# Optimization experiments

Hardware: AMD Instinct MI355X
Metric: run time of the kernel (lower is better)

Reference implementation:

```python
import jax, jax.numpy as jnp
import numpy as np

H = 20  # hidden size (hard-coded in the module)

def setup_inputs() -> dict:
    key = jax.random.key(0)
    ks = jax.random.split(key, 7)
    B, T = 4096, 1000
    s = 1.0 / np.sqrt(H)  # torch default init bound for RNN/Linear
    x = jax.random.normal(ks[0], (B, T, 1), dtype=jnp.float32)
    W_ih = jax.random.uniform(ks[1], (H, 1), jnp.float32, -s, s)
    W_hh = jax.random.uniform(ks[2], (H, H), jnp.float32, -s, s)
    b_ih = jax.random.uniform(ks[3], (H,), jnp.float32, -s, s)
    b_hh = jax.random.uniform(ks[4], (H,), jnp.float32, -s, s)
    fc_w = jax.random.uniform(ks[5], (1, H), jnp.float32, -s, s)
    fc_b = jax.random.uniform(ks[6], (1,), jnp.float32, -s, s)
    return {"x": x, "W_ih": W_ih, "W_hh": W_hh, "b_ih": b_ih,
            "b_hh": b_hh, "fc_w": fc_w, "fc_b": fc_b}

def reference(x, W_ih, W_hh, b_ih, b_hh, fc_w, fc_b):
    # x: [B, T, 1] -> time-major [T, B, 1] for scan
    B = x.shape[0]
    xt = jnp.swapaxes(x, 0, 1)
    # precompute input projection for all timesteps: [T, B, H]
    xproj = jnp.einsum('tbi,hi->tbh', xt, W_ih) + b_ih + b_hh
    h0 = jnp.zeros((B, H), dtype=x.dtype)
    def step(h, xp_t):
        h_new = jax.nn.relu(xp_t + h @ W_hh.T)
        return h_new, None
    h_last, _ = jax.lax.scan(step, h0, xproj)
    # only the last hidden state feeds the head: fc1(rnn_out[:, -1, :])
    out = h_last @ fc_w.T + fc_b  # [B, 1]
    return out
```

## Files before the change

kernel.cpp:

```cpp
#include <hip/hip_runtime.h>


#define TT 1000

typedef float v2f __attribute__((ext_vector_type(2)));

struct Col { v2f p01, p23; float v4; };

struct Init { v2f i01, i23; float i4; };

#define PIN(v)  asm volatile("" : "+v"(v))
__device__ __forceinline__ void pinc(Col& c) {
    PIN(c.p01); PIN(c.p23); PIN(c.v4);
}
__device__ __forceinline__ void keepc(const Col& c) {
    asm volatile("" :: "v"(c.p01), "v"(c.p23), "v"(c.v4));
}

template <int CTRL>
__device__ __forceinline__ float dpp_f(float v) {
    return __int_as_float(__builtin_amdgcn_update_dpp(
        0, __float_as_int(v), CTRL, 0xF, 0xF, true));
}

#define QP_XOR1 0xB1
#define QP_XOR2 0x4E
#define ROR4   0x124
#define ROR8   0x128

__device__ __forceinline__ Init mkinit(v2f xs, float xt,
                                       const Col& w, const Col& b) {
    Init r;
    r.i01 = __builtin_elementwise_fma(xs, w.p01, b.p01);
    r.i23 = __builtin_elementwise_fma(xs, w.p23, b.p23);
    r.i4  = __builtin_fmaf(xt, w.v4, b.v4);
    return r;
}

template <int C1, int C2>
__device__ __forceinline__ void step(const Init& in,
                                     v2f& h01, v2f& h23, float& h4,
                                     const Col& wc0, const Col& wc1,
                                     const Col& wc2, const Col& wc3,
                                     const Col& wc4) {
    v2f  X01 = __builtin_elementwise_fma(h01.xx, wc0.p01, in.i01);
    v2f  X23 = __builtin_elementwise_fma(h01.xx, wc0.p23, in.i23);
    float x4 = __builtin_fmaf(h01.x, wc0.v4, in.i4);
    X01 = __builtin_elementwise_fma(h01.yy, wc1.p01, X01);
    X23 = __builtin_elementwise_fma(h01.yy, wc1.p23, X23);
    x4  = __builtin_fmaf(h01.y, wc1.v4, x4);

    v2f  Y01 = h23.xx * wc2.p01;
    v2f  Y23 = h23.xx * wc2.p23;
    float y4 = h23.x * wc2.v4;
    Y01 = __builtin_elementwise_fma(h23.yy, wc3.p01, Y01);
    Y23 = __builtin_elementwise_fma(h23.yy, wc3.p23, Y23);
    y4  = __builtin_fmaf(h23.y, wc3.v4, y4);
    { const v2f h4s = {h4, h4};
      Y01 = __builtin_elementwise_fma(h4s, wc4.p01, Y01);
      Y23 = __builtin_elementwise_fma(h4s, wc4.p23, Y23);
      y4  = __builtin_fmaf(h4, wc4.v4, y4); }

    const v2f z = {0.f, 0.f};

    {
        v2f A = X01 + Y01;
        float b0 = A.x, b1 = A.y;
        float t0 = dpp_f<C1>(b0), t1 = dpp_f<C1>(b1);
        b0 += t0; b1 += t1;
        t0 = dpp_f<C2>(b0); t1 = dpp_f<C2>(b1);
        b0 += t0; b1 += t1;
        v2f r = {b0, b1};
        h01 = __builtin_elementwise_max(r, z);
    }
    {
        v2f A = X23 + Y23;
        float b2 = A.x, b3 = A.y;
        float t2 = dpp_f<C1>(b2), t3 = dpp_f<C1>(b3);
        b2 += t2; b3 += t3;
        t2 = dpp_f<C2>(b2); t3 = dpp_f<C2>(b3);
        b2 += t2; b3 += t3;
        v2f r = {b2, b3};
        h23 = __builtin_elementwise_max(r, z);
    }
    {
        float b4 = x4 + y4;
        float t4 = dpp_f<C1>(b4); b4 += t4;
        t4 = dpp_f<C2>(b4); b4 += t4;
        h4 = fmaxf(b4, 0.f);
    }
}

__global__ void
__attribute__((amdgpu_flat_work_group_size(64, 64), amdgpu_waves_per_eu(1, 1)))
rnn_os_kernel(const float* __restrict__ x,
              const float* __restrict__ W_ih,
              const float* __restrict__ W_hh,
              const float* __restrict__ b_ih,
              const float* __restrict__ b_hh,
              const float* __restrict__ fc_w,
              const float* __restrict__ fc_b,
              float* __restrict__ out) {
    const int tid = blockIdx.x * 64 + threadIdx.x;
    const int b   = tid >> 4;
    const int gl  = tid & 15;
    const int a   = gl >> 2;
    const int bq  = gl & 3;

    Col we0, we1, we2, we3, we4;
    Col wo0, wo1, wo2, wo3, wo4;
#define LOADC(wk, k, rbase, cbase)                                            \
    { (wk).p01 = (v2f){ W_hh[((rbase) + 0) * 20 + (cbase) + (k)],             \
                        W_hh[((rbase) + 1) * 20 + (cbase) + (k)] };           \
      (wk).p23 = (v2f){ W_hh[((rbase) + 2) * 20 + (cbase) + (k)],             \
                        W_hh[((rbase) + 3) * 20 + (cbase) + (k)] };           \
      (wk).v4  =        W_hh[((rbase) + 4) * 20 + (cbase) + (k)]; }
    LOADC(we0, 0, a * 5, bq * 5) LOADC(we1, 1, a * 5, bq * 5)
    LOADC(we2, 2, a * 5, bq * 5) LOADC(we3, 3, a * 5, bq * 5)
    LOADC(we4, 4, a * 5, bq * 5)
    LOADC(wo0, 0, bq * 5, a * 5) LOADC(wo1, 1, bq * 5, a * 5)
    LOADC(wo2, 2, bq * 5, a * 5) LOADC(wo3, 3, bq * 5, a * 5)
    LOADC(wo4, 4, bq * 5, a * 5)
#undef LOADC

    const bool eact = (bq == 0);
    const bool oact = (a == 0);
    Col wie, bie, wio, bio;
#define LOADIB(wv, bv, base, act)                                             \
    { const float* pw = W_ih + (base);                                        \
      const float* p1 = b_ih + (base);                                        \
      const float* p2 = b_hh + (base);                                        \
      (wv).p01 = (v2f){ (act) ? pw[0] : 0.f, (act) ? pw[1] : 0.f };           \
      (wv).p23 = (v2f){ (act) ? pw[2] : 0.f, (act) ? pw[3] : 0.f };           \
      (wv).v4  =        (act) ? pw[4] : 0.f;                                  \
      (bv).p01 = (v2f){ (act) ? (p1[0] + p2[0]) : 0.f,                        \
                        (act) ? (p1[1] + p2[1]) : 0.f };                      \
      (bv).p23 = (v2f){ (act) ? (p1[2] + p2[2]) : 0.f,                        \
                        (act) ? (p1[3] + p2[3]) : 0.f };                      \
      (bv).v4  =        (act) ? (p1[4] + p2[4]) : 0.f; }
    LOADIB(wie, bie, a * 5,  eact)
    LOADIB(wio, bio, bq * 5, oact)
#undef LOADIB

    pinc(we0); pinc(we1); pinc(we2); pinc(we3); pinc(we4);
    pinc(wo0); pinc(wo1); pinc(wo2); pinc(wo3); pinc(wo4);
    pinc(wie); pinc(bie); pinc(wio); pinc(bio);

    v2f h01 = {0.f, 0.f}, h23 = {0.f, 0.f};
    float h4 = 0.f;

    const float* __restrict__ xb = x + (size_t)b * TT;

#define LOAD5(P, off)                                   \
    P##0 = *(const float4*)(xb + (off));                \
    P##1 = *(const float4*)(xb + (off) + 4);            \
    P##2 = *(const float4*)(xb + (off) + 8);            \
    P##3 = *(const float4*)(xb + (off) + 12);           \
    P##4 = *(const float4*)(xb + (off) + 16);

#define STEP_E(I) step<QP_XOR1, QP_XOR2>(I, h01, h23, h4, we0, we1, we2, we3, we4);
#define STEP_O(I) step<ROR4,    ROR8   >(I, h01, h23, h4, wo0, wo1, wo2, wo3, wo4);
#define RUN4(Q) {                                       \
        const v2f qlo = {Q.x, Q.y};                     \
        const v2f qhi = {Q.z, Q.w};                     \
        const Init iEL = mkinit(qlo.xx, qlo.x, wie, bie); \
        const Init iOL = mkinit(qlo.yy, qlo.y, wio, bio); \
        const Init iEH = mkinit(qhi.xx, qhi.x, wie, bie); \
        const Init iOH = mkinit(qhi.yy, qhi.y, wio, bio); \
        STEP_E(iEL) STEP_O(iOL)                         \
        STEP_E(iEH) STEP_O(iOH) }
#define RUN20(P) RUN4(P##0) RUN4(P##1) RUN4(P##2) RUN4(P##3) RUN4(P##4)

    float4 A0, A1, A2, A3, A4;
    float4 B0, B1, B2, B3, B4;
    LOAD5(A, 0)
    LOAD5(B, 20)

    for (int it = 0; it < 24; ++it) {
        const int base = it * 40;
        RUN20(A)
        LOAD5(A, base + 40)
        RUN20(B)
        LOAD5(B, base + 60)
    }
    RUN20(A)
    RUN20(B)

#undef RUN20
#undef RUN4
#undef STEP_E
#undef STEP_O
#undef LOAD5

    keepc(we0); keepc(we1); keepc(we2); keepc(we3); keepc(we4);
    keepc(wo0); keepc(wo1); keepc(wo2); keepc(wo3); keepc(wo4);
    keepc(wie); keepc(bie); keepc(wio); keepc(bio);

    float dot;
    {
        const float* pf = fc_w + bq * 5;
        float f0 = oact ? pf[0] : 0.f, f1 = oact ? pf[1] : 0.f;
        float f2 = oact ? pf[2] : 0.f, f3 = oact ? pf[3] : 0.f;
        float f4 = oact ? pf[4] : 0.f;
        dot = h01.x * f0;
        dot = __builtin_fmaf(h01.y, f1, dot);
        dot = __builtin_fmaf(h23.x, f2, dot);
        dot = __builtin_fmaf(h23.y, f3, dot);
        dot = __builtin_fmaf(h4,    f4, dot);
    }
    dot += __shfl_xor(dot, 1, 16);
    dot += __shfl_xor(dot, 2, 16);
    dot += __shfl_xor(dot, 4, 16);
    dot += __shfl_xor(dot, 8, 16);

    if (gl == 0)
        out[b] = dot + fc_b[0];
}

extern "C" void kernel_launch(void* const* d_in, const int* in_sizes, int n_in,
                              void* d_out, int out_size, void* d_ws, size_t ws_size,
                              hipStream_t stream) {
    const float* x    = (const float*)d_in[0];
    const float* W_ih = (const float*)d_in[1];
    const float* W_hh = (const float*)d_in[2];
    const float* b_ih = (const float*)d_in[3];
    const float* b_hh = (const float*)d_in[4];
    const float* fc_w = (const float*)d_in[5];
    const float* fc_b = (const float*)d_in[6];
    float* out = (float*)d_out;

    const int block = 64;
    const int grid  = (4096 * 16) / block;
    rnn_os_kernel<<<grid, block, 0, stream>>>(x, W_ih, W_hh, b_ih, b_hh,
                                              fc_w, fc_b, out);
}
```

Before: 152.2 us.

## Use eight lanes per batch row with bpermute hidden-state redistribution

```diff
diff --git a/kernel.cpp b/kernel.cpp
--- a/kernel.cpp
+++ b/kernel.cpp
@@ -17,19 +17,17 @@
     asm volatile("" :: "v"(c.p01), "v"(c.p23), "v"(c.v4));
 }
 
-template <int CTRL>
-__device__ __forceinline__ float dpp_f(float v) {
+__device__ __forceinline__ float dpp_xor1(float v) {
     return __int_as_float(__builtin_amdgcn_update_dpp(
-        0, __float_as_int(v), CTRL, 0xF, 0xF, true));
-}
-
-#define QP_XOR1 0xB1
-#define QP_XOR2 0x4E
-#define ROR4   0x124
-#define ROR8   0x128
-
-__device__ __forceinline__ Init mkinit(v2f xs, float xt,
-                                       const Col& w, const Col& b) {
+        0, __float_as_int(v), 0xB1, 0xF, 0xF, true));
+}
+
+__device__ __forceinline__ float bpf(int addr, float v) {
+    return __int_as_float(__builtin_amdgcn_ds_bpermute(addr, __float_as_int(v)));
+}
+
+__device__ __forceinline__ Init mkinit(float xt, const Col& w, const Col& b) {
+    const v2f xs = {xt, xt};
     Init r;
     r.i01 = __builtin_elementwise_fma(xs, w.p01, b.p01);
     r.i23 = __builtin_elementwise_fma(xs, w.p23, b.p23);
@@ -37,57 +35,72 @@
     return r;
 }
 
-template <int C1, int C2>
 __device__ __forceinline__ void step(const Init& in,
-                                     v2f& h01, v2f& h23, float& h4,
-                                     const Col& wc0, const Col& wc1,
-                                     const Col& wc2, const Col& wc3,
-                                     const Col& wc4) {
-    v2f  X01 = __builtin_elementwise_fma(h01.xx, wc0.p01, in.i01);
-    v2f  X23 = __builtin_elementwise_fma(h01.xx, wc0.p23, in.i23);
-    float x4 = __builtin_fmaf(h01.x, wc0.v4, in.i4);
-    X01 = __builtin_elementwise_fma(h01.yy, wc1.p01, X01);
-    X23 = __builtin_elementwise_fma(h01.yy, wc1.p23, X23);
-    x4  = __builtin_fmaf(h01.y, wc1.v4, x4);
-
-    v2f  Y01 = h23.xx * wc2.p01;
-    v2f  Y23 = h23.xx * wc2.p23;
-    float y4 = h23.x * wc2.v4;
-    Y01 = __builtin_elementwise_fma(h23.yy, wc3.p01, Y01);
-    Y23 = __builtin_elementwise_fma(h23.yy, wc3.p23, Y23);
-    y4  = __builtin_fmaf(h23.y, wc3.v4, y4);
-    { const v2f h4s = {h4, h4};
-      Y01 = __builtin_elementwise_fma(h4s, wc4.p01, Y01);
-      Y23 = __builtin_elementwise_fma(h4s, wc4.p23, Y23);
-      y4  = __builtin_fmaf(h4, wc4.v4, y4); }
+    v2f& h01, v2f& h23, float& h4,
+    v2f& hA01, v2f& hA23, float& hA4,
+    v2f& hB01, v2f& hB23, float& hB4,
+    int addrA, int addrB,
+    const Col& c0, const Col& c1, const Col& c2, const Col& c3, const Col& c4,
+    const Col& c5, const Col& c6, const Col& c7, const Col& c8, const Col& c9)
+{
+    v2f  X01 = __builtin_elementwise_fma(hA01.xx, c0.p01, in.i01);
+    v2f  X23 = __builtin_elementwise_fma(hA01.xx, c0.p23, in.i23);
+    float x4 = __builtin_fmaf(hA01.x, c0.v4, in.i4);
+    X01 = __builtin_elementwise_fma(hA01.yy, c1.p01, X01);
+    X23 = __builtin_elementwise_fma(hA01.yy, c1.p23, X23);
+    x4  = __builtin_fmaf(hA01.y, c1.v4, x4);
+    X01 = __builtin_elementwise_fma(hA23.xx, c2.p01, X01);
+    X23 = __builtin_elementwise_fma(hA23.xx, c2.p23, X23);
+    x4  = __builtin_fmaf(hA23.x, c2.v4, x4);
+    X01 = __builtin_elementwise_fma(hA23.yy, c3.p01, X01);
+    X23 = __builtin_elementwise_fma(hA23.yy, c3.p23, X23);
+    x4  = __builtin_fmaf(hA23.y, c3.v4, x4);
+    { const v2f s = {hA4, hA4};
+      X01 = __builtin_elementwise_fma(s, c4.p01, X01);
+      X23 = __builtin_elementwise_fma(s, c4.p23, X23);
+      x4  = __builtin_fmaf(hA4, c4.v4, x4); }
+
+    v2f  Y01 = hB01.xx * c5.p01;
+    v2f  Y23 = hB01.xx * c5.p23;
+    float y4 = hB01.x * c5.v4;
+    Y01 = __builtin_elementwise_fma(hB01.yy, c6.p01, Y01);
+    Y23 = __builtin_elementwise_fma(hB01.yy, c6.p23, Y23);
+    y4  = __builtin_fmaf(hB01.y, c6.v4, y4);
+    Y01 = __builtin_elementwise_fma(hB23.xx, c7.p01, Y01);
+    Y23 = __builtin_elementwise_fma(hB23.xx, c7.p23, Y23);
+    y4  = __builtin_fmaf(hB23.x, c7.v4, y4);
+    Y01 = __builtin_elementwise_fma(hB23.yy, c8.p01, Y01);
+    Y23 = __builtin_elementwise_fma(hB23.yy, c8.p23, Y23);
+    y4  = __builtin_fmaf(hB23.y, c8.v4, y4);
+    { const v2f s = {hB4, hB4};
+      Y01 = __builtin_elementwise_fma(s, c9.p01, Y01);
+      Y23 = __builtin_elementwise_fma(s, c9.p23, Y23);
+      y4  = __builtin_fmaf(hB4, c9.v4, y4); }
 
     const v2f z = {0.f, 0.f};
 
     {
         v2f A = X01 + Y01;
-        float b0 = A.x, b1 = A.y;
-        float t0 = dpp_f<C1>(b0), t1 = dpp_f<C1>(b1);
-        b0 += t0; b1 += t1;
-        t0 = dpp_f<C2>(b0); t1 = dpp_f<C2>(b1);
-        b0 += t0; b1 += t1;
-        v2f r = {b0, b1};
+        float t0 = dpp_xor1(A.x), t1 = dpp_xor1(A.y);
+        v2f r = {A.x + t0, A.y + t1};
         h01 = __builtin_elementwise_max(r, z);
+        hA01 = (v2f){ bpf(addrA, h01.x), bpf(addrA, h01.y) };
+        hB01 = (v2f){ bpf(addrB, h01.x), bpf(addrB, h01.y) };
     }
     {
         v2f A = X23 + Y23;
-        float b2 = A.x, b3 = A.y;
-        float t2 = dpp_f<C1>(b2), t3 = dpp_f<C1>(b3);
-        b2 += t2; b3 += t3;
-        t2 = dpp_f<C2>(b2); t3 = dpp_f<C2>(b3);
-        b2 += t2; b3 += t3;
-        v2f r = {b2, b3};
+        float t2 = dpp_xor1(A.x), t3 = dpp_xor1(A.y);
+        v2f r = {A.x + t2, A.y + t3};
         h23 = __builtin_elementwise_max(r, z);
+        hA23 = (v2f){ bpf(addrA, h23.x), bpf(addrA, h23.y) };
+        hB23 = (v2f){ bpf(addrB, h23.x), bpf(addrB, h23.y) };
     }
     {
         float b4 = x4 + y4;
-        float t4 = dpp_f<C1>(b4); b4 += t4;
-        t4 = dpp_f<C2>(b4); b4 += t4;
-        h4 = fmaxf(b4, 0.f);
+        float t4 = dpp_xor1(b4);
+        h4 = fmaxf(b4 + t4, 0.f);
+        hA4 = bpf(addrA, h4);
+        hB4 = bpf(addrB, h4);
     }
 }
 
@@ -102,52 +115,54 @@
               const float* __restrict__ fc_b,
               float* __restrict__ out) {
     const int tid = blockIdx.x * 64 + threadIdx.x;
-    const int b   = tid >> 4;
-    const int gl  = tid & 15;
-    const int a   = gl >> 2;
-    const int bq  = gl & 3;
-
-    Col we0, we1, we2, we3, we4;
-    Col wo0, wo1, wo2, wo3, wo4;
-#define LOADC(wk, k, rbase, cbase)                                            \
-    { (wk).p01 = (v2f){ W_hh[((rbase) + 0) * 20 + (cbase) + (k)],             \
-                        W_hh[((rbase) + 1) * 20 + (cbase) + (k)] };           \
-      (wk).p23 = (v2f){ W_hh[((rbase) + 2) * 20 + (cbase) + (k)],             \
-                        W_hh[((rbase) + 3) * 20 + (cbase) + (k)] };           \
-      (wk).v4  =        W_hh[((rbase) + 4) * 20 + (cbase) + (k)]; }
-    LOADC(we0, 0, a * 5, bq * 5) LOADC(we1, 1, a * 5, bq * 5)
-    LOADC(we2, 2, a * 5, bq * 5) LOADC(we3, 3, a * 5, bq * 5)
-    LOADC(we4, 4, a * 5, bq * 5)
-    LOADC(wo0, 0, bq * 5, a * 5) LOADC(wo1, 1, bq * 5, a * 5)
-    LOADC(wo2, 2, bq * 5, a * 5) LOADC(wo3, 3, bq * 5, a * 5)
-    LOADC(wo4, 4, bq * 5, a * 5)
+    const int b   = tid >> 3;
+    const int j   = tid & 7;
+    const int a   = j >> 1;
+    const int kh  = j & 1;
+
+    const int l      = threadIdx.x;
+    const int srcA   = (l & ~7) | (kh << 2);
+    const int addrA  = srcA << 2;
+    const int addrB  = addrA + 8;
+
+    Col c0, c1, c2, c3, c4, c5, c6, c7, c8, c9;
+#define LOADC(ck, k)                                                          \
+    { const int col = kh * 10 + (k);                                          \
+      (ck).p01 = (v2f){ W_hh[(a * 5 + 0) * 20 + col],                         \
+                        W_hh[(a * 5 + 1) * 20 + col] };                       \
+      (ck).p23 = (v2f){ W_hh[(a * 5 + 2) * 20 + col],                         \
+                        W_hh[(a * 5 + 3) * 20 + col] };                       \
+      (ck).v4  =        W_hh[(a * 5 + 4) * 20 + col]; }
+    LOADC(c0, 0) LOADC(c1, 1) LOADC(c2, 2) LOADC(c3, 3) LOADC(c4, 4)
+    LOADC(c5, 5) LOADC(c6, 6) LOADC(c7, 7) LOADC(c8, 8) LOADC(c9, 9)
 #undef LOADC
 
-    const bool eact = (bq == 0);
-    const bool oact = (a == 0);
-    Col wie, bie, wio, bio;
-#define LOADIB(wv, bv, base, act)                                             \
-    { const float* pw = W_ih + (base);                                        \
-      const float* p1 = b_ih + (base);                                        \
-      const float* p2 = b_hh + (base);                                        \
-      (wv).p01 = (v2f){ (act) ? pw[0] : 0.f, (act) ? pw[1] : 0.f };           \
-      (wv).p23 = (v2f){ (act) ? pw[2] : 0.f, (act) ? pw[3] : 0.f };           \
-      (wv).v4  =        (act) ? pw[4] : 0.f;                                  \
-      (bv).p01 = (v2f){ (act) ? (p1[0] + p2[0]) : 0.f,                        \
-                        (act) ? (p1[1] + p2[1]) : 0.f };                      \
-      (bv).p23 = (v2f){ (act) ? (p1[2] + p2[2]) : 0.f,                        \
-                        (act) ? (p1[3] + p2[3]) : 0.f };                      \
-      (bv).v4  =        (act) ? (p1[4] + p2[4]) : 0.f; }
-    LOADIB(wie, bie, a * 5,  eact)
-    LOADIB(wio, bio, bq * 5, oact)
-#undef LOADIB
-
-    pinc(we0); pinc(we1); pinc(we2); pinc(we3); pinc(we4);
-    pinc(wo0); pinc(wo1); pinc(wo2); pinc(wo3); pinc(wo4);
-    pinc(wie); pinc(bie); pinc(wio); pinc(bio);
+    const bool act = (kh == 0);
+    Col wie, bie;
+    {
+        const float* pw = W_ih + a * 5;
+        const float* p1 = b_ih + a * 5;
+        const float* p2 = b_hh + a * 5;
+        wie.p01 = (v2f){ act ? pw[0] : 0.f, act ? pw[1] : 0.f };
+        wie.p23 = (v2f){ act ? pw[2] : 0.f, act ? pw[3] : 0.f };
+        wie.v4  =        act ? pw[4] : 0.f;
+        bie.p01 = (v2f){ act ? (p1[0] + p2[0]) : 0.f,
+                         act ? (p1[1] + p2[1]) : 0.f };
+        bie.p23 = (v2f){ act ? (p1[2] + p2[2]) : 0.f,
+                         act ? (p1[3] + p2[3]) : 0.f };
+        bie.v4  =        act ? (p1[4] + p2[4]) : 0.f;
+    }
+
+    pinc(c0); pinc(c1); pinc(c2); pinc(c3); pinc(c4);
+    pinc(c5); pinc(c6); pinc(c7); pinc(c8); pinc(c9);
+    pinc(wie); pinc(bie);
 
     v2f h01 = {0.f, 0.f}, h23 = {0.f, 0.f};
     float h4 = 0.f;
+    v2f hA01 = {0.f, 0.f}, hA23 = {0.f, 0.f};
+    float hA4 = 0.f;
+    v2f hB01 = {0.f, 0.f}, hB23 = {0.f, 0.f};
+    float hB4 = 0.f;
 
     const float* __restrict__ xb = x + (size_t)b * TT;
 
@@ -158,17 +173,11 @@
     P##3 = *(const float4*)(xb + (off) + 12);           \
     P##4 = *(const float4*)(xb + (off) + 16);
 
-#define STEP_E(I) step<QP_XOR1, QP_XOR2>(I, h01, h23, h4, we0, we1, we2, we3, we4);
-#define STEP_O(I) step<ROR4,    ROR8   >(I, h01, h23, h4, wo0, wo1, wo2, wo3, wo4);
-#define RUN4(Q) {                                       \
-        const v2f qlo = {Q.x, Q.y};                     \
-        const v2f qhi = {Q.z, Q.w};                     \
-        const Init iEL = mkinit(qlo.xx, qlo.x, wie, bie); \
-        const Init iOL = mkinit(qlo.yy, qlo.y, wio, bio); \
-        const Init iEH = mkinit(qhi.xx, qhi.x, wie, bie); \
-        const Init iOH = mkinit(qhi.yy, qhi.y, wio, bio); \
-        STEP_E(iEL) STEP_O(iOL)                         \
-        STEP_E(iEH) STEP_O(iOH) }
+#define STEP1(XT) {                                                        \
+        const Init in_ = mkinit((XT), wie, bie);                           \
+        step(in_, h01, h23, h4, hA01, hA23, hA4, hB01, hB23, hB4,          \
+             addrA, addrB, c0, c1, c2, c3, c4, c5, c6, c7, c8, c9); }
+#define RUN4(Q) { STEP1(Q.x) STEP1(Q.y) STEP1(Q.z) STEP1(Q.w) }
 #define RUN20(P) RUN4(P##0) RUN4(P##1) RUN4(P##2) RUN4(P##3) RUN4(P##4)
 
     float4 A0, A1, A2, A3, A4;
@@ -188,32 +197,30 @@
 
 #undef RUN20
 #undef RUN4
-#undef STEP_E
-#undef STEP_O
+#undef STEP1
 #undef LOAD5
 
-    keepc(we0); keepc(we1); keepc(we2); keepc(we3); keepc(we4);
-    keepc(wo0); keepc(wo1); keepc(wo2); keepc(wo3); keepc(wo4);
-    keepc(wie); keepc(bie); keepc(wio); keepc(bio);
+    keepc(c0); keepc(c1); keepc(c2); keepc(c3); keepc(c4);
+    keepc(c5); keepc(c6); keepc(c7); keepc(c8); keepc(c9);
+    keepc(wie); keepc(bie);
 
     float dot;
     {
-        const float* pf = fc_w + bq * 5;
-        float f0 = oact ? pf[0] : 0.f, f1 = oact ? pf[1] : 0.f;
-        float f2 = oact ? pf[2] : 0.f, f3 = oact ? pf[3] : 0.f;
-        float f4 = oact ? pf[4] : 0.f;
+        const float* pf = fc_w + a * 5;
+        float f0 = act ? pf[0] : 0.f, f1 = act ? pf[1] : 0.f;
+        float f2 = act ? pf[2] : 0.f, f3 = act ? pf[3] : 0.f;
+        float f4 = act ? pf[4] : 0.f;
         dot = h01.x * f0;
         dot = __builtin_fmaf(h01.y, f1, dot);
         dot = __builtin_fmaf(h23.x, f2, dot);
         dot = __builtin_fmaf(h23.y, f3, dot);
         dot = __builtin_fmaf(h4,    f4, dot);
     }
-    dot += __shfl_xor(dot, 1, 16);
-    dot += __shfl_xor(dot, 2, 16);
-    dot += __shfl_xor(dot, 4, 16);
-    dot += __shfl_xor(dot, 8, 16);
-
-    if (gl == 0)
+    dot += __shfl_xor(dot, 1, 8);
+    dot += __shfl_xor(dot, 2, 8);
+    dot += __shfl_xor(dot, 4, 8);
+
+    if (j == 0)
         out[b] = dot + fc_b[0];
 }
 
@@ -230,7 +237,7 @@
     float* out = (float*)d_out;
 
     const int block = 64;
-    const int grid  = (4096 * 16) / block;
+    const int grid  = (4096 * 8) / block;
     rnn_os_kernel<<<grid, block, 0, stream>>>(x, W_ih, W_hh, b_ih, b_hh,
                                               fc_w, fc_b, out);
 }
```

After: 236.1 us. 1.55x slower.
